# Kernel optimization log

Measured on AMD Instinct MI355X. Metric: run time of the kernel, lower is better.

## Reference

```python
import jax, jax.numpy as jnp
import numpy as np

D_MAIN = 256
D_INT = 512
N_FEAT = 128
N_CLASSES = 10
B = 1024
N_CAND = 100000
CTX = 96
EPS = 1e-5


def layer_norm(x, scale, bias):
    m = jnp.mean(x, axis=-1, keepdims=True)
    v = jnp.var(x, axis=-1, keepdims=True)
    return (x - m) / jnp.sqrt(v + EPS) * scale + bias


def setup_inputs() -> dict:
    key = jax.random.key(0)
    ks = jax.random.split(key, 16)

    def lin_w(k, fi, fo):
        return jax.random.uniform(k, (fi, fo), minval=-1.0, maxval=1.0, dtype=jnp.float32) / np.sqrt(fi)

    def lin_b(k, fi, fo):
        return jax.random.uniform(k, (fo,), minval=-1.0, maxval=1.0, dtype=jnp.float32) / np.sqrt(fi)

    return {
        "x_num": jax.random.normal(ks[0], (B, N_FEAT), dtype=jnp.float32),
        "cand_num": jax.random.normal(ks[1], (N_CAND, N_FEAT), dtype=jnp.float32),
        "cand_y": jax.random.randint(ks[2], (N_CAND,), 0, N_CLASSES),
        "context_size": CTX,
        # input linear (forward_E with encoder_n_blocks=0)
        "W_lin": lin_w(ks[3], N_FEAT, D_MAIN), "b_lin": lin_b(ks[3], N_FEAT, D_MAIN),
        # K projection
        "W_K": lin_w(ks[4], D_MAIN, D_MAIN), "b_K": lin_b(ks[4], D_MAIN, D_MAIN),
        # label embedding Y (init uniform(-1, 1) per reset_parameters)
        "Y_emb": jax.random.uniform(ks[5], (N_CLASSES, D_MAIN), minval=-1.0, maxval=1.0, dtype=jnp.float32),
        # T: Linear(d, d_int) -> ReLU -> Linear(d_int, d, bias=False)
        "T_W1": lin_w(ks[6], D_MAIN, D_INT), "T_b1": lin_b(ks[6], D_MAIN, D_INT),
        "T_W2": lin_w(ks[7], D_INT, D_MAIN),
        # predictor block (LayerNorm -> Linear -> ReLU -> Dropout -> Linear), residual
        "bp_ln_s": jnp.ones((D_MAIN,), jnp.float32), "bp_ln_b": jnp.zeros((D_MAIN,), jnp.float32),
        "bp_W1": lin_w(ks[8], D_MAIN, D_INT), "bp_b1": lin_b(ks[8], D_MAIN, D_INT),
        "bp_W2": lin_w(ks[9], D_INT, D_MAIN), "bp_b2": lin_b(ks[9], D_INT, D_MAIN),
        # head P: LayerNorm -> ReLU -> Linear(d, n_classes)
        "P_ln_s": jnp.ones((D_MAIN,), jnp.float32), "P_ln_b": jnp.zeros((D_MAIN,), jnp.float32),
        "P_W": lin_w(ks[10], D_MAIN, N_CLASSES), "P_b": lin_b(ks[10], D_MAIN, N_CLASSES),
    }


def reference(x_num, cand_num, cand_y, context_size,
              W_lin, b_lin, W_K, b_K, Y_emb, T_W1, T_b1, T_W2,
              bp_ln_s, bp_ln_b, bp_W1, bp_b1, bp_W2, bp_b2,
              P_ln_s, P_ln_b, P_W, P_b):
    # forward_E (encoder_n_blocks=0 => single Linear, normlization is None)
    x = x_num @ W_lin + b_lin                       # [B, d]
    k = x @ W_K + b_K                               # [B, d]

    # candidate keys computed under torch.no_grad in the original -> stop_gradient
    ki_all = jax.lax.stop_gradient((cand_num @ W_lin + b_lin) @ W_K + b_K)  # [N, d]

    # FAISS GpuIndexFlatL2 search: exact L2 top-k (smallest squared distance)
    d2 = (jnp.sum(k * k, axis=-1, keepdims=True)
          - 2.0 * (k @ ki_all.T)
          + jnp.sum(ki_all * ki_all, axis=-1))      # [B, N]
    _, I = jax.lax.top_k(-jax.lax.stop_gradient(d2), context_size)  # [B, C]

    ki = ki_all[I]                                  # [B, C, d]
    diff = k[:, None, :] - ki                       # [B, C, d]
    # NOTE: source computes S = -(-|k|^2 + 2 k.ki - |ki|^2) = +squared distance
    S = jnp.sum(diff * diff, axis=-1)               # [B, C]
    w = jax.nn.softmax(S, axis=-1)                  # context_dropout inactive at inference

    enc_y = Y_emb[cand_y[I]]                        # [B, C, d]
    V = enc_y + jax.nn.relu(diff @ T_W1 + T_b1) @ T_W2
    V = jnp.einsum('bc,bcd->bd', w, V)              # weighted aggregation

    x = x + V
    # predictor block (predictor_n_blocks=1)
    h = layer_norm(x, bp_ln_s, bp_ln_b)
    h = jax.nn.relu(h @ bp_W1 + bp_b1) @ bp_W2 + bp_b2
    x = x + h
    # head P
    return jax.nn.relu(layer_norm(x, P_ln_s, P_ln_b)) @ P_W + P_b
```

## Files before the change

kernel.cpp:

```cpp
#include <hip/hip_runtime.h>
#include <hip/hip_bf16.h>

#define B_ROWS   1024
#define N_FEAT   128
#define D_MAIN   256
#define D_INT    512
#define N_CAND   100000
#define CTX      96
#define N_CLS    10
#define PCHN     8192
#define N2       91808
#define RKEEP    128
#define SCAP     6144
#define MH       50000
#define SVSTRIDE 16

typedef __attribute__((ext_vector_type(8))) short bf16x8;
typedef __attribute__((ext_vector_type(4))) float f32x4;
typedef unsigned long long u64;

__device__ __forceinline__ float wsum(float v) {
    #pragma unroll
    for (int o = 32; o > 0; o >>= 1) v += __shfl_down(v, o);
    return v;
}
__device__ __forceinline__ float wmax(float v) {
    #pragma unroll
    for (int o = 32; o > 0; o >>= 1) v = fmaxf(v, __shfl_down(v, o));
    return v;
}
__device__ __forceinline__ float blockSum256(float v, float* red) {
    int t = threadIdx.x;
    float s = wsum(v);
    if ((t & 63) == 0) red[t >> 6] = s;
    __syncthreads();
    s = red[0] + red[1] + red[2] + red[3];
    __syncthreads();
    return s;
}
__device__ __forceinline__ float b2f(unsigned short u) {
    return __uint_as_float(((unsigned)u) << 16);
}
__device__ __forceinline__ unsigned short f2b(float f) {
    unsigned x = __float_as_uint(f);
    return (unsigned short)((x + 0x7fff + ((x >> 16) & 1)) >> 16);
}
__device__ __forceinline__ unsigned fkey(float f) {
    unsigned u = __float_as_uint(f);
    return u ^ ((((int)u >> 31)) | 0x80000000u);
}
__device__ __forceinline__ float finv(unsigned k) {
    unsigned u = (k & 0x80000000u) ? (k ^ 0x80000000u) : ~k;
    return __uint_as_float(u);
}
#define SPLIT1(x, hv, lv) { unsigned short _h = f2b(x); hv = (short)_h; lv = (short)f2b((x) - b2f(_h)); }

__global__ __launch_bounds__(256) void encode_batch(
    const float* __restrict__ xn, const float* __restrict__ Wl, const float* __restrict__ bl,
    const float* __restrict__ Wk, const float* __restrict__ bk,
    float* __restrict__ xout, float* __restrict__ kout, float* __restrict__ knorm)
{
    int b = blockIdx.x, t = threadIdx.x;
    __shared__ float si[128], sx[256], red[4];
    if (t < 128) si[t] = xn[b * N_FEAT + t];
    __syncthreads();
    float a = bl[t];
    for (int i = 0; i < 128; ++i) a += si[i] * Wl[i * D_MAIN + t];
    xout[b * D_MAIN + t] = a;
    sx[t] = a;
    __syncthreads();
    float a2 = bk[t];
    for (int i = 0; i < 256; ++i) a2 += sx[i] * Wk[i * D_MAIN + t];
    kout[b * D_MAIN + t] = a2;
    float s = blockSum256(a2 * a2, red);
    if (t == 0) knorm[b] = s;
}

template<bool WRITE_BF16>
__global__ __launch_bounds__(256) void gemm_split3(
    const float* __restrict__ A,
    const unsigned short* __restrict__ Bh,
    const unsigned short* __restrict__ Bl,
    const float* __restrict__ bias,
    float* __restrict__ Cf,
    unsigned short* __restrict__ Cbf,
    int M, int N, int K)
{
    __shared__ __align__(16) short Ash[4096], Asl[4096], Bsh[4096], Bsl[4096];
    const int t = threadIdx.x;
    const int bm = blockIdx.x * 128, bn = blockIdx.y * 128;
    const int wave = t >> 6, lane = t & 63;
    const int wm = (wave >> 1) * 64, wn = (wave & 1) * 64;
    const int lr = lane & 15, lkg = lane >> 4;
    f32x4 acc[4][4] = {};
    const int row0 = t >> 2, kg0 = t & 3;
    const int row1 = row0 + 64;
    const int p0 = ((kg0 + (row0 >> 2)) & 3) ^ (row0 & 3);
    const int p1 = ((kg0 + (row1 >> 2)) & 3) ^ (row1 & 3);
    const int gm0 = bm + row0, gm1 = bm + row1;
    const int n0r = bn + row0, n1r = bn + row1;

    float4 u00, u01, u10, u11;
    bf16x8 b0h, b0l, b1h, b1l;
    auto prefetch = [&](int kq) {
        float4 z4 = make_float4(0.f, 0.f, 0.f, 0.f); bf16x8 z = {};
        u00 = z4; u01 = z4; u10 = z4; u11 = z4;
        b0h = z; b0l = z; b1h = z; b1l = z;
        if (gm0 < M) {
            const float* ap = A + (size_t)gm0 * K + kq + kg0 * 8;
            u00 = *(const float4*)ap; u01 = *(const float4*)(ap + 4);
        }
        if (gm1 < M) {
            const float* ap = A + (size_t)gm1 * K + kq + kg0 * 8;
            u10 = *(const float4*)ap; u11 = *(const float4*)(ap + 4);
        }
        if (n0r < N) {
            b0h = *(const bf16x8*)(Bh + (size_t)n0r * K + kq + kg0 * 8);
            b0l = *(const bf16x8*)(Bl + (size_t)n0r * K + kq + kg0 * 8);
        }
        if (n1r < N) {
            b1h = *(const bf16x8*)(Bh + (size_t)n1r * K + kq + kg0 * 8);
            b1l = *(const bf16x8*)(Bl + (size_t)n1r * K + kq + kg0 * 8);
        }
    };
    prefetch(0);

    for (int k0 = 0; k0 < K; k0 += 32) {
        bf16x8 a0h, a0l, a1h, a1l;
        SPLIT1(u00.x, a0h[0], a0l[0]); SPLIT1(u00.y, a0h[1], a0l[1]);
        SPLIT1(u00.z, a0h[2], a0l[2]); SPLIT1(u00.w, a0h[3], a0l[3]);
        SPLIT1(u01.x, a0h[4], a0l[4]); SPLIT1(u01.y, a0h[5], a0l[5]);
        SPLIT1(u01.z, a0h[6], a0l[6]); SPLIT1(u01.w, a0h[7], a0l[7]);
        SPLIT1(u10.x, a1h[0], a1l[0]); SPLIT1(u10.y, a1h[1], a1l[1]);
        SPLIT1(u10.z, a1h[2], a1l[2]); SPLIT1(u10.w, a1h[3], a1l[3]);
        SPLIT1(u11.x, a1h[4], a1l[4]); SPLIT1(u11.y, a1h[5], a1l[5]);
        SPLIT1(u11.z, a1h[6], a1l[6]); SPLIT1(u11.w, a1h[7], a1l[7]);
        __syncthreads();
        *(bf16x8*)&Ash[(row0 * 4 + p0) * 8] = a0h;
        *(bf16x8*)&Asl[(row0 * 4 + p0) * 8] = a0l;
        *(bf16x8*)&Ash[(row1 * 4 + p1) * 8] = a1h;
        *(bf16x8*)&Asl[(row1 * 4 + p1) * 8] = a1l;
        *(bf16x8*)&Bsh[(row0 * 4 + p0) * 8] = b0h;
        *(bf16x8*)&Bsl[(row0 * 4 + p0) * 8] = b0l;
        *(bf16x8*)&Bsh[(row1 * 4 + p1) * 8] = b1h;
        *(bf16x8*)&Bsl[(row1 * 4 + p1) * 8] = b1l;
        if (k0 + 32 < K) prefetch(k0 + 32);
        __syncthreads();
        bf16x8 ah[4], al[4], bh[4], blo[4];
        #pragma unroll
        for (int m = 0; m < 4; ++m) {
            int r = wm + m * 16 + lr;
            int p = ((lkg + (r >> 2)) & 3) ^ (r & 3);
            ah[m] = *(const bf16x8*)&Ash[(r * 4 + p) * 8];
            al[m] = *(const bf16x8*)&Asl[(r * 4 + p) * 8];
        }
        #pragma unroll
        for (int n = 0; n < 4; ++n) {
            int r = wn + n * 16 + lr;
            int p = ((lkg + (r >> 2)) & 3) ^ (r & 3);
            bh[n] = *(const bf16x8*)&Bsh[(r * 4 + p) * 8];
            blo[n] = *(const bf16x8*)&Bsl[(r * 4 + p) * 8];
        }
        #pragma unroll
        for (int m = 0; m < 4; ++m)
            #pragma unroll
            for (int n = 0; n < 4; ++n) {
                acc[m][n] = __builtin_amdgcn_mfma_f32_16x16x32_bf16(al[m], bh[n], acc[m][n], 0, 0, 0);
                acc[m][n] = __builtin_amdgcn_mfma_f32_16x16x32_bf16(ah[m], blo[n], acc[m][n], 0, 0, 0);
                acc[m][n] = __builtin_amdgcn_mfma_f32_16x16x32_bf16(ah[m], bh[n], acc[m][n], 0, 0, 0);
            }
    }
    #pragma unroll
    for (int m = 0; m < 4; ++m) {
        #pragma unroll
        for (int n = 0; n < 4; ++n) {
            f32x4 a = acc[m][n];
            int gcol = bn + wn + n * 16 + lr;
            if (gcol >= N) continue;
            float bv = bias[gcol];
            #pragma unroll
            for (int r = 0; r < 4; ++r) {
                int grow = bm + wm + m * 16 + lkg * 4 + r;
                if (grow >= M) continue;
                float v = a[r] + bv;
                Cf[(size_t)grow * N + gcol] = v;
                if (WRITE_BF16) Cbf[(size_t)grow * N + gcol] = f2b(v);
            }
        }
    }
}

template<bool RELU, bool OUT_BF16>
__global__ __launch_bounds__(256) void gemm_bf16(
    const unsigned short* __restrict__ A,
    const unsigned short* __restrict__ Bt,
    const float* __restrict__ bias,
    void* __restrict__ C, int M, int N, int K)
{
    __shared__ __align__(16) short As[4096];
    __shared__ __align__(16) short Bs[2048];
    const int t = threadIdx.x;
    const int bm = blockIdx.x * 128, bn = blockIdx.y * 64;
    const int wave = t >> 6, lane = t & 63;
    const int wm = (wave >> 1) * 64, wn = (wave & 1) * 32;
    const int lr = lane & 15, lkg = lane >> 4;
    f32x4 acc[4][2] = {};
    const int row0 = t >> 2, kg0 = t & 3;
    const int row1 = row0 + 64;
    const int p0 = ((kg0 + (row0 >> 2)) & 3) ^ (row0 & 3);
    const int p1 = ((kg0 + (row1 >> 2)) & 3) ^ (row1 & 3);
    const int gm0 = bm + row0, gm1 = bm + row1;
    const int nB = bn + row0;

    bf16x8 a0, a1, b0;
    auto prefetch = [&](int kq) {
        bf16x8 z = {};
        a0 = z; a1 = z; b0 = z;
        if (gm0 < M) a0 = *(const bf16x8*)(A + (size_t)gm0 * K + kq + kg0 * 8);
        if (gm1 < M) a1 = *(const bf16x8*)(A + (size_t)gm1 * K + kq + kg0 * 8);
        if (row0 < 64 && nB < N) b0 = *(const bf16x8*)(Bt + (size_t)nB * K + kq + kg0 * 8);
    };
    prefetch(0);

    for (int k0 = 0; k0 < K; k0 += 32) {
        __syncthreads();
        *(bf16x8*)&As[(row0 * 4 + p0) * 8] = a0;
        *(bf16x8*)&As[(row1 * 4 + p1) * 8] = a1;
        if (row0 < 64) *(bf16x8*)&Bs[(row0 * 4 + p0) * 8] = b0;
        if (k0 + 32 < K) prefetch(k0 + 32);
        __syncthreads();
        bf16x8 bfr[2];
        #pragma unroll
        for (int n = 0; n < 2; ++n) {
            int r = wn + n * 16 + lr;
            int p = ((lkg + (r >> 2)) & 3) ^ (r & 3);
            bfr[n] = *(const bf16x8*)&Bs[(r * 4 + p) * 8];
        }
        #pragma unroll
        for (int m = 0; m < 4; ++m) {
            int r = wm + m * 16 + lr;
            int p = ((lkg + (r >> 2)) & 3) ^ (r & 3);
            bf16x8 af = *(const bf16x8*)&As[(r * 4 + p) * 8];
            #pragma unroll
            for (int n = 0; n < 2; ++n)
                acc[m][n] = __builtin_amdgcn_mfma_f32_16x16x32_bf16(
                    af, bfr[n], acc[m][n], 0, 0, 0);
        }
    }
    #pragma unroll
    for (int m = 0; m < 4; ++m) {
        #pragma unroll
        for (int n = 0; n < 2; ++n) {
            f32x4 a = acc[m][n];
            int gcol = bn + wn + n * 16 + lr;
            if (gcol >= N) continue;
            float bv = bias ? bias[gcol] : 0.f;
            #pragma unroll
            for (int r = 0; r < 4; ++r) {
                int grow = bm + wm + m * 16 + lkg * 4 + r;
                if (grow >= M) continue;
                float v = a[r] + bv;
                if (RELU) v = fmaxf(v, 0.f);
                if (OUT_BF16)
                    ((unsigned short*)C)[(size_t)grow * N + gcol] = f2b(v);
                else
                    ((float*)C)[(size_t)grow * N + gcol] = v;
            }
        }
    }
}

template<int MODE>
__global__ __launch_bounds__(256) void screen_gemm(
    const unsigned short* __restrict__ A,
    const unsigned short* __restrict__ Bt,
    float* __restrict__ scores,
    int N, int n0,
    const float* __restrict__ knrm,
    const unsigned* __restrict__ tau32, int* __restrict__ svcnt,
    u64* __restrict__ surv)
{
    __shared__ __align__(16) short As[4096];
    __shared__ __align__(16) short Bs[2048];
    const int t = threadIdx.x;
    const int bm = blockIdx.x * 128, bn = blockIdx.y * 64;
    const int wave = t >> 6, lane = t & 63;
    const int wm = (wave >> 1) * 64, wn = (wave & 1) * 32;
    const int lr = lane & 15, lkg = lane >> 4;
    f32x4 acc[4][2] = {};
    const int row0 = t >> 2, kg0 = t & 3;
    const int row1 = row0 + 64;
    const int p0 = ((kg0 + (row0 >> 2)) & 3) ^ (row0 & 3);
    const int p1 = ((kg0 + (row1 >> 2)) & 3) ^ (row1 & 3);
    const int gm0 = bm + row0, gm1 = bm + row1;
    const int nB = bn + row0;

    bf16x8 a0, a1, b0;
    auto prefetch = [&](int kq) {
        bf16x8 z = {};
        b0 = z;
        a0 = *(const bf16x8*)(A + (size_t)gm0 * D_MAIN + kq + kg0 * 8);
        a1 = *(const bf16x8*)(A + (size_t)gm1 * D_MAIN + kq + kg0 * 8);
        if (row0 < 64 && nB < N) b0 = *(const bf16x8*)(Bt + (size_t)nB * D_MAIN + kq + kg0 * 8);
    };
    prefetch(0);

    for (int k0 = 0; k0 < D_MAIN; k0 += 32) {
        __syncthreads();
        *(bf16x8*)&As[(row0 * 4 + p0) * 8] = a0;
        *(bf16x8*)&As[(row1 * 4 + p1) * 8] = a1;
        if (row0 < 64) *(bf16x8*)&Bs[(row0 * 4 + p0) * 8] = b0;
        if (k0 + 32 < D_MAIN) prefetch(k0 + 32);
        __syncthreads();
        bf16x8 bfr[2];
        #pragma unroll
        for (int n = 0; n < 2; ++n) {
            int r = wn + n * 16 + lr;
            int p = ((lkg + (r >> 2)) & 3) ^ (r & 3);
            bfr[n] = *(const bf16x8*)&Bs[(r * 4 + p) * 8];
        }
        #pragma unroll
        for (int m = 0; m < 4; ++m) {
            int r = wm + m * 16 + lr;
            int p = ((lkg + (r >> 2)) & 3) ^ (r & 3);
            bf16x8 af = *(const bf16x8*)&As[(r * 4 + p) * 8];
            #pragma unroll
            for (int n = 0; n < 2; ++n)
                acc[m][n] = __builtin_amdgcn_mfma_f32_16x16x32_bf16(
                    af, bfr[n], acc[m][n], 0, 0, 0);
        }
    }

    float knv[2];
    #pragma unroll
    for (int n = 0; n < 2; ++n) {
        int gcol = bn + wn + n * 16 + lr;
        knv[n] = (gcol < N) ? knrm[gcol] : 0.f;
    }
    if (MODE == 1) {
        #pragma unroll
        for (int m = 0; m < 4; ++m) {
            #pragma unroll
            for (int n = 0; n < 2; ++n) {
                int gcol = bn + wn + n * 16 + lr;
                if (gcol >= N) continue;
                #pragma unroll
                for (int r = 0; r < 4; ++r) {
                    int grow = bm + wm + m * 16 + lkg * 4 + r;
                    scores[(size_t)grow * PCHN + gcol] = knv[n] - 2.0f * acc[m][n][r];
                }
            }
        }
    } else {
        unsigned taur[16];
        #pragma unroll
        for (int m = 0; m < 4; ++m)
            #pragma unroll
            for (int r = 0; r < 4; ++r)
                taur[m * 4 + r] = tau32[bm + wm + m * 16 + lkg * 4 + r];
        #pragma unroll
        for (int m = 0; m < 4; ++m) {
            #pragma unroll
            for (int r = 0; r < 4; ++r) {
                int grow = bm + wm + m * 16 + lkg * 4 + r;
                #pragma unroll
                for (int n = 0; n < 2; ++n) {
                    int gcol = bn + wn + n * 16 + lr;
                    bool pass = false;
                    unsigned key = 0;
                    if (gcol < N) {
                        key = fkey(knv[n] - 2.0f * acc[m][n][r]);
                        pass = key <= taur[m * 4 + r];
                    }
                    u64 bal = __ballot(pass);
                    unsigned g16 = (unsigned)((bal >> (lkg * 16)) & 0xFFFFu);
                    if (g16) {
                        int cntp = __popc(g16);
                        int first = __ffs(g16) - 1;
                        int base = 0;
                        if (lr == first) base = atomicAdd(&svcnt[grow * SVSTRIDE], cntp);
                        base = __shfl(base, lkg * 16 + first);
                        if (pass) {
                            int p = base + __popc(g16 & ((1u << lr) - 1u));
                            if (p < SCAP)
                                surv[(size_t)grow * SCAP + p] =
                                    ((u64)key << 32) | (unsigned)(n0 + gcol);
                        }
                    }
                }
            }
        }
    }
}

__global__ __launch_bounds__(256) void cvt_f32_bf16_vec(
    const float* __restrict__ in, unsigned short* __restrict__ out, int n4)
{
    int i = blockIdx.x * 256 + threadIdx.x;
    if (i >= n4) return;
    float4 v = ((const float4*)in)[i];
    ushort4 u;
    u.x = f2b(v.x); u.y = f2b(v.y); u.z = f2b(v.z); u.w = f2b(v.w);
    ((ushort4*)out)[i] = u;
}
__global__ __launch_bounds__(256) void cvt_transpose(
    const float* __restrict__ W, unsigned short* __restrict__ Wt, int K, int N)
{
    int idx = blockIdx.x * 256 + threadIdx.x;
    if (idx >= K * N) return;
    int k = idx / N, n = idx % N;
    Wt[(size_t)n * K + k] = f2b(W[idx]);
}
__global__ __launch_bounds__(256) void cvt_split_transpose(
    const float* __restrict__ W, unsigned short* __restrict__ Wh,
    unsigned short* __restrict__ Wl, int K, int N)
{
    int idx = blockIdx.x * 256 + threadIdx.x;
    if (idx >= K * N) return;
    int k = idx / N, n = idx % N;
    float v = W[idx];
    unsigned short h = f2b(v);
    Wh[(size_t)n * K + k] = h;
    Wl[(size_t)n * K + k] = f2b(v - b2f(h));
}

__global__ __launch_bounds__(256) void rownorms(const float* __restrict__ ki,
                                                float* __restrict__ out, int M)
{
    int n = blockIdx.x * 4 + (threadIdx.x >> 6);
    int lane = threadIdx.x & 63;
    if (n >= M) return;
    float4 v = *(const float4*)(ki + (size_t)n * D_MAIN + lane * 4);
    float s = v.x * v.x + v.y * v.y + v.z * v.z + v.w * v.w;
    s = wsum(s);
    if (lane == 0) out[n] = s;
}

__device__ void bitonic512(u64* s, int t)
{
    for (int k = 2; k <= 512; k <<= 1) {
        for (int j = k >> 1; j > 0; j >>= 1) {
            __syncthreads();
            #pragma unroll
            for (int q = 0; q < 2; ++q) {
                int l = t + q * 256;
                int p = l ^ j;
                if (p > l) {
                    u64 a = s[l], bb = s[p];
                    bool up = ((l & k) == 0);
                    if ((a > bb) == up) { s[l] = bb; s[p] = a; }
                }
            }
        }
    }
    __syncthreads();
}
__device__ void bitonic1024(u64* s, int t)
{
    for (int k = 2; k <= 1024; k <<= 1) {
        for (int j = k >> 1; j > 0; j >>= 1) {
            __syncthreads();
            #pragma unroll
            for (int q = 0; q < 4; ++q) {
                int l = t + q * 256;
                int p = l ^ j;
                if (p > l) {
                    u64 a = s[l], bb = s[p];
                    bool up = ((l & k) == 0);
                    if ((a > bb) == up) { s[l] = bb; s[p] = a; }
                }
            }
        }
    }
    __syncthreads();
}

__global__ __launch_bounds__(256) void pilot_select(
    const float* __restrict__ scores, u64* __restrict__ pilotbuf,
    unsigned* __restrict__ tau32)
{
    int b = blockIdx.x, t = threadIdx.x;
    int lane = t & 63;
    __shared__ u64 s[1024];
    __shared__ int cnt;
    __shared__ u64 tauf;
    const float* row = scores + (size_t)b * PCHN;
    #pragma unroll
    for (int q = 0; q < 4; ++q) {
        int n = t + q * 256;
        s[n] = ((u64)fkey(row[n]) << 32) | (unsigned)n;
    }
    __syncthreads();
    bitonic1024(s, t);
    if (t == 0) { cnt = 128; tauf = s[127]; }
    #pragma unroll
    for (int q = 0; q < 4; ++q) { int n = t + q * 256; if (n >= 128) s[n] = ~0ULL; }
    __syncthreads();
    for (int base = 1024; base < PCHN; base += 1024) {
        u64 tau = tauf;
        int n = base + t * 4;
        float4 v = *(const float4*)(row + n);
        #pragma unroll
        for (int j = 0; j < 4; ++j) {
            float x = (&v.x)[j];
            u64 e = ((u64)fkey(x) << 32) | (unsigned)(n + j);
            bool pass = e < tau;
            u64 m = __ballot(pass);
            if (m) {
                int bs = 0;
                if (lane == 0) bs = atomicAdd(&cnt, (int)__popcll(m));
                bs = __shfl(bs, 0);
                if (pass) {
                    int p = bs + (int)__popcll(m & ((1ULL << lane) - 1ULL));
                    if (p < 1024) s[p] = e;
                }
            }
        }
        __syncthreads();
        if (cnt > 512) {
            bitonic1024(s, t);
            if (t == 0) { cnt = 128; tauf = s[127]; }
            #pragma unroll
            for (int q = 0; q < 4; ++q) { int n2 = t + q * 256; if (n2 >= 128) s[n2] = ~0ULL; }
        }
        __syncthreads();
    }
    bitonic1024(s, t);
    if (t < 128) pilotbuf[(size_t)b * 128 + t] = s[t];
    if (t == 0) tau32[b] = (unsigned)(s[127] >> 32);
}

__global__ __launch_bounds__(128) void init_surv(
    const u64* __restrict__ pilotbuf, u64* __restrict__ surv, int* __restrict__ svcnt)
{
    int b = blockIdx.x, t = threadIdx.x;
    surv[(size_t)b * SCAP + t] = pilotbuf[(size_t)b * 128 + t];
    if (t == 0) svcnt[b * SVSTRIDE] = 128;
}

__global__ __launch_bounds__(256) void final_select(
    const u64* __restrict__ surv, const int* __restrict__ svcnt,
    int* __restrict__ refI)
{
    int b = blockIdx.x, t = threadIdx.x;
    int lane = t & 63;
    __shared__ u64 s[1024];
    __shared__ int cnt;
    __shared__ u64 tauf;
    int total = svcnt[b * SVSTRIDE]; if (total > SCAP) total = SCAP;
    const u64* rowp = surv + (size_t)b * SCAP;
    #pragma unroll
    for (int q = 0; q < 4; ++q) {
        int n = t + q * 256;
        s[n] = (n < total) ? rowp[n] : ~0ULL;
    }
    __syncthreads();
    bitonic1024(s, t);
    if (t == 0) { cnt = 128; tauf = s[127]; }
    #pragma unroll
    for (int q = 0; q < 4; ++q) { int n = t + q * 256; if (n >= 128) s[n] = ~0ULL; }
    __syncthreads();
    for (int base = 1024; base < total; base += 1024) {
        u64 tau = tauf;
        int n = base + t * 4;
        #pragma unroll
        for (int j = 0; j < 4; ++j) {
            u64 e = (n + j < total) ? rowp[n + j] : ~0ULL;
            bool pass = e < tau;
            u64 m = __ballot(pass);
            if (m) {
                int bs = 0;
                if (lane == 0) bs = atomicAdd(&cnt, (int)__popcll(m));
                bs = __shfl(bs, 0);
                if (pass) {
                    int p = bs + (int)__popcll(m & ((1ULL << lane) - 1ULL));
                    if (p < 1024) s[p] = e;
                }
            }
        }
        __syncthreads();
        if (cnt > 512) {
            bitonic1024(s, t);
            if (t == 0) { cnt = 128; tauf = s[127]; }
            #pragma unroll
            for (int q = 0; q < 4; ++q) { int n2 = t + q * 256; if (n2 >= 128) s[n2] = ~0ULL; }
        }
        __syncthreads();
    }
    bitonic1024(s, t);
    if (t < RKEEP) refI[b * RKEEP + t] = (int)(unsigned)(s[t] & 0xffffffffULL);
}

__global__ __launch_bounds__(256) void refine(
    const float* __restrict__ kmat, const float* __restrict__ kiall,
    const float* __restrict__ knorm, const float* __restrict__ kinorm,
    const int* __restrict__ refI, int* __restrict__ Ifin, float* __restrict__ Sbuf)
{
    int b = blockIdx.x, t = threadIdx.x;
    int w = t >> 6, lane = t & 63;
    __shared__ float kk[256];
    __shared__ u64 s[512];
    kk[t] = kmat[b * D_MAIN + t];
    s[t] = ~0ULL; s[t + 256] = ~0ULL;
    __syncthreads();
    float kn = knorm[b];
    for (int sv = w; sv < RKEEP; sv += 4) {
        int n = refI[b * RKEEP + sv];
        float4 a = *(const float4*)&kk[lane * 4];
        float4 bb = ((const float4*)(kiall + (size_t)n * D_MAIN))[lane];
        float d = a.x * bb.x + a.y * bb.y + a.z * bb.z + a.w * bb.w;
        d = wsum(d);
        if (lane == 0) {
            float d2 = kn + kinorm[n] - 2.f * d;
            s[sv] = ((u64)fkey(d2) << 32) | (unsigned)n;
        }
    }
    __syncthreads();
    bitonic512(s, t);
    if (t < CTX) {
        u64 e = s[t];
        Ifin[b * CTX + t] = (int)(unsigned)(e & 0xffffffffULL);
        Sbuf[b * CTX + t] = finv((unsigned)(e >> 32));
    }
}

__global__ __launch_bounds__(64) void gather_diff_bf(
    const float* __restrict__ kmat, const float* __restrict__ kiall,
    const int* __restrict__ I, unsigned short* __restrict__ diffb)
{
    int bc = blockIdx.x;
    int b = bc / CTX;
    int t = threadIdx.x;
    int idx = I[bc];
    float4 kv = ((const float4*)(kmat + (size_t)b * D_MAIN))[t];
    float4 iv = ((const float4*)(kiall + (size_t)idx * D_MAIN))[t];
    ushort4 u;
    u.x = f2b(kv.x - iv.x); u.y = f2b(kv.y - iv.y);
    u.z = f2b(kv.z - iv.z); u.w = f2b(kv.w - iv.w);
    ((ushort4*)(diffb + (size_t)bc * D_MAIN))[t] = u;
}

__global__ __launch_bounds__(128) void softmax96(const float* __restrict__ S,
                                                 float* __restrict__ w)
{
    int b = blockIdx.x, t = threadIdx.x;
    __shared__ float rm[2], rs[2];
    float v = (t < CTX) ? S[b * CTX + t] : -__builtin_inff();
    float m = wmax(v);
    if ((t & 63) == 0) rm[t >> 6] = m;
    __syncthreads();
    m = fmaxf(rm[0], rm[1]);
    float e = (t < CTX) ? expf(v - m) : 0.f;
    float ss = wsum(e);
    if ((t & 63) == 0) rs[t >> 6] = ss;
    __syncthreads();
    float Z = rs[0] + rs[1];
    if (t < CTX) w[b * CTX + t] = e / Z;
}

__global__ __launch_bounds__(256) void aggregate(
    const float* __restrict__ w, const int* __restrict__ I,
    const int* __restrict__ cand_y, const float* __restrict__ Yemb,
    const float* __restrict__ mlp, const float* __restrict__ x,
    float* __restrict__ x2)
{
    int b = blockIdx.x, t = threadIdx.x;
    __shared__ float ws[CTX];
    __shared__ int lab[CTX];
    if (t < CTX) {
        ws[t] = w[b * CTX + t];
        lab[t] = cand_y[I[b * CTX + t]];
    }
    __syncthreads();
    float acc = 0.f;
    for (int c = 0; c < CTX; ++c) {
        acc += ws[c] * (Yemb[lab[c] * D_MAIN + t] + mlp[((size_t)b * CTX + c) * D_MAIN + t]);
    }
    x2[b * D_MAIN + t] = x[b * D_MAIN + t] + acc;
}

__global__ __launch_bounds__(256) void predictor_head(
    const float* __restrict__ x2,
    const float* __restrict__ lns, const float* __restrict__ lnb,
    const float* __restrict__ W1, const float* __restrict__ b1,
    const float* __restrict__ W2, const float* __restrict__ b2,
    const float* __restrict__ plns, const float* __restrict__ plnb,
    const float* __restrict__ PW, const float* __restrict__ Pb,
    float* __restrict__ out)
{
    int b = blockIdx.x, t = threadIdx.x;
    __shared__ float ln1[256], hdn[512], red[4];
    float xv = x2[b * D_MAIN + t];
    float s1 = blockSum256(xv, red);
    float s2 = blockSum256(xv * xv, red);
    float mean = s1 * (1.f / 256.f);
    float var = s2 * (1.f / 256.f) - mean * mean;
    float rstd = rsqrtf(var + 1e-5f);
    ln1[t] = (xv - mean) * rstd * lns[t] + lnb[t];
    __syncthreads();
    #pragma unroll
    for (int rep = 0; rep < 2; ++rep) {
        int j = t + rep * 256;
        float a = b1[j];
        for (int i = 0; i < 256; ++i) a += ln1[i] * W1[i * D_INT + j];
        hdn[j] = fmaxf(a, 0.f);
    }
    __syncthreads();
    float a3 = b2[t];
    for (int i = 0; i < 512; ++i) a3 += hdn[i] * W2[i * D_MAIN + t];
    float x3 = xv + a3;
    float s3 = blockSum256(x3, red);
    float s4 = blockSum256(x3 * x3, red);
    float m2 = s3 * (1.f / 256.f);
    float v2 = s4 * (1.f / 256.f) - m2 * m2;
    float r2 = rsqrtf(v2 + 1e-5f);
    float rv = fmaxf((x3 - m2) * r2 * plns[t] + plnb[t], 0.f);
    __syncthreads();
    ln1[t] = rv;
    __syncthreads();
    if (t < N_CLS) {
        float a = Pb[t];
        for (int i = 0; i < 256; ++i) a += ln1[i] * PW[i * N_CLS + t];
        out[b * N_CLS + t] = a;
    }
}

extern "C" void kernel_launch(void* const* d_in, const int* in_sizes, int n_in,
                              void* d_out, int out_size, void* d_ws, size_t ws_size,
                              hipStream_t stream)
{
    (void)in_sizes; (void)n_in; (void)out_size; (void)ws_size;
    const float* x_num   = (const float*)d_in[0];
    const float* cand    = (const float*)d_in[1];
    const int*   cand_y  = (const int*)d_in[2];
    const float* W_lin   = (const float*)d_in[4];
    const float* b_lin   = (const float*)d_in[5];
    const float* W_K     = (const float*)d_in[6];
    const float* b_K     = (const float*)d_in[7];
    const float* Y_emb   = (const float*)d_in[8];
    const float* T_W1    = (const float*)d_in[9];
    const float* T_b1    = (const float*)d_in[10];
    const float* T_W2    = (const float*)d_in[11];
    const float* bp_ln_s = (const float*)d_in[12];
    const float* bp_ln_b = (const float*)d_in[13];
    const float* bp_W1   = (const float*)d_in[14];
    const float* bp_b1   = (const float*)d_in[15];
    const float* bp_W2   = (const float*)d_in[16];
    const float* bp_b2   = (const float*)d_in[17];
    const float* P_ln_s  = (const float*)d_in[18];
    const float* P_ln_b  = (const float*)d_in[19];
    const float* P_W     = (const float*)d_in[20];
    const float* P_b     = (const float*)d_in[21];
    float* outp = (float*)d_out;

    char* ws = (char*)d_ws;
    float* kiall  = (float*)(ws + 0);
    unsigned short* hidden = (unsigned short*)(ws + 0);
    unsigned short* ki_bf = (unsigned short*)(ws + 102400000);
    unsigned short* diffb = (unsigned short*)(ws + 102400000);
    float* mlpbuf = (float*)(ws + 102400000);
    float* hcand  = (float*)(ws + 153600000);
    float* scores = (float*)(ws + 153600000);
    u64*   surv   = (u64*)(ws + 153600000);
    const size_t T = 204800000;
    float* xbuf   = (float*)(ws + T + 0);
    float* kbuf   = (float*)(ws + T + 1048576);
    float* x2buf  = (float*)(ws + T + 2097152);
    float* knorm  = (float*)(ws + T + 3145728);
    float* kinorm = (float*)(ws + T + 3149824);
    unsigned short* k_bf = (unsigned short*)(ws + T + 3551232);
    unsigned short* Wlh  = (unsigned short*)(ws + T + 4075520);
    unsigned short* Wll  = (unsigned short*)(ws + T + 4141056);
    unsigned short* Wkh  = (unsigned short*)(ws + T + 4206592);
    unsigned short* Wkl  = (unsigned short*)(ws + T + 4337664);
    unsigned short* W1t  = (unsigned short*)(ws + T + 4468736);
    unsigned short* W2t  = (unsigned short*)(ws + T + 4730880);
    float* Sbuf   = (float*)(ws + T + 4993024);
    float* wbuf   = (float*)(ws + T + 5386240);
    int*   refI   = (int*)(ws + T + 5779456);
    int*   Ifin   = (int*)(ws + T + 6303744);
    u64*   pilotbuf = (u64*)(ws + T + 6696960);
    unsigned* tau32 = (unsigned*)(ws + T + 7745536);
    int*   svcnt  = (int*)(ws + T + 7749632);

    encode_batch<<<B_ROWS, 256, 0, stream>>>(x_num, W_lin, b_lin, W_K, b_K,
                                             xbuf, kbuf, knorm);
    cvt_split_transpose<<<128, 256, 0, stream>>>(W_lin, Wlh, Wll, N_FEAT, D_MAIN);
    cvt_split_transpose<<<256, 256, 0, stream>>>(W_K, Wkh, Wkl, D_MAIN, D_MAIN);
    cvt_transpose<<<512, 256, 0, stream>>>(T_W1, W1t, D_MAIN, D_INT);
    cvt_transpose<<<512, 256, 0, stream>>>(T_W2, W2t, D_INT, D_MAIN);
    cvt_f32_bf16_vec<<<256, 256, 0, stream>>>(kbuf, k_bf, B_ROWS * D_MAIN / 4);
    for (int h = 0; h < 2; ++h) {
        gemm_split3<false><<<dim3(391, 2), 256, 0, stream>>>(
            cand + (size_t)h * MH * N_FEAT, Wlh, Wll, b_lin,
            hcand, nullptr, MH, D_MAIN, N_FEAT);
        gemm_split3<true><<<dim3(391, 2), 256, 0, stream>>>(
            hcand, Wkh, Wkl, b_K,
            kiall + (size_t)h * MH * D_MAIN, ki_bf + (size_t)h * MH * D_MAIN,
            MH, D_MAIN, D_MAIN);
    }
    rownorms<<<25000, 256, 0, stream>>>(kiall, kinorm, N_CAND);
    screen_gemm<1><<<dim3(8, PCHN / 64), 256, 0, stream>>>(
        k_bf, ki_bf, scores, PCHN, 0, kinorm, nullptr, nullptr, nullptr);
    pilot_select<<<B_ROWS, 256, 0, stream>>>(scores, pilotbuf, tau32);
    init_surv<<<B_ROWS, 128, 0, stream>>>(pilotbuf, surv, svcnt);
    screen_gemm<2><<<dim3(8, (N2 + 63) / 64), 256, 0, stream>>>(
        k_bf, ki_bf + (size_t)PCHN * D_MAIN, nullptr, N2, PCHN,
        kinorm + PCHN, tau32, svcnt, surv);
    final_select<<<B_ROWS, 256, 0, stream>>>(surv, svcnt, refI);
    refine<<<B_ROWS, 256, 0, stream>>>(kbuf, kiall, knorm, kinorm, refI, Ifin, Sbuf);
    softmax96<<<B_ROWS, 128, 0, stream>>>(Sbuf, wbuf);
    gather_diff_bf<<<B_ROWS * CTX, 64, 0, stream>>>(kbuf, kiall, Ifin, diffb);
    gemm_bf16<true, true><<<dim3(768, 8), 256, 0, stream>>>(
        diffb, W1t, T_b1, hidden, B_ROWS * CTX, D_INT, D_MAIN);
    gemm_bf16<false, false><<<dim3(768, 4), 256, 0, stream>>>(
        hidden, W2t, nullptr, mlpbuf, B_ROWS * CTX, D_MAIN, D_INT);
    aggregate<<<B_ROWS, 256, 0, stream>>>(wbuf, Ifin, cand_y, Y_emb, mlpbuf,
                                          xbuf, x2buf);
    predictor_head<<<B_ROWS, 256, 0, stream>>>(x2buf, bp_ln_s, bp_ln_b,
                                               bp_W1, bp_b1, bp_W2, bp_b2,
                                               P_ln_s, P_ln_b, P_W, P_b, outp);
}
```

Before: 936.2 us.

## Fold input and K projections into one fused weight for candidate encoding

Precomputes W_lin@W_K and b_lin@W_K+b_K on device, so the candidate keys come from a single 128-K split-bf16 GEMM instead of two chained GEMMs with an fp32 intermediate. This removes the hcand write and read and about two thirds of the candidate-encoding FLOPs. The split3 GEMM tile narrows to 128x64, and the bf16 GEMMs drop a row guard on B loads. Reassociating the product changes rounding slightly, which could in rare cases reorder near-tie neighbours in the top-k.

```diff
diff --git a/kernel.cpp b/kernel.cpp
--- a/kernel.cpp
+++ b/kernel.cpp
@@ -12,7 +12,6 @@
 #define N2       91808
 #define RKEEP    128
 #define SCAP     6144
-#define MH       50000
 #define SVSTRIDE 16
 
 typedef __attribute__((ext_vector_type(8))) short bf16x8;
@@ -74,6 +73,32 @@
     kout[b * D_MAIN + t] = a2;
     float s = blockSum256(a2 * a2, red);
     if (t == 0) knorm[b] = s;
+}
+
+__global__ __launch_bounds__(256) void fuse_weights(
+    const float* __restrict__ Wl, const float* __restrict__ Wk,
+    const float* __restrict__ bl, const float* __restrict__ bk,
+    float* __restrict__ Wf, float* __restrict__ bf)
+{
+    int i = blockIdx.x, t = threadIdx.x;
+    __shared__ float row[256];
+    if (i < 128) {
+        if (t < 128) row[t] = 0.f;
+        row[t % 256] = 0.f;
+        __syncthreads();
+        if (t < 256) {  }
+        row[t] = Wl[i * D_MAIN + t];
+        __syncthreads();
+        float a = 0.f;
+        for (int k = 0; k < 256; ++k) a += row[k] * Wk[k * D_MAIN + t];
+        Wf[i * D_MAIN + t] = a;
+    } else {
+        row[t] = bl[t];
+        __syncthreads();
+        float a = bk[t];
+        for (int k = 0; k < 256; ++k) a += row[k] * Wk[k * D_MAIN + t];
+        bf[t] = a;
+    }
 }
 
 template<bool WRITE_BF16>
@@ -86,26 +111,27 @@
     unsigned short* __restrict__ Cbf,
     int M, int N, int K)
 {
-    __shared__ __align__(16) short Ash[4096], Asl[4096], Bsh[4096], Bsl[4096];
+    __shared__ __align__(16) short Ash[4096], Asl[4096];
+    __shared__ __align__(16) short Bsh[2048], Bsl[2048];
     const int t = threadIdx.x;
-    const int bm = blockIdx.x * 128, bn = blockIdx.y * 128;
+    const int bm = blockIdx.x * 128, bn = blockIdx.y * 64;
     const int wave = t >> 6, lane = t & 63;
-    const int wm = (wave >> 1) * 64, wn = (wave & 1) * 64;
+    const int wm = (wave >> 1) * 64, wn = (wave & 1) * 32;
     const int lr = lane & 15, lkg = lane >> 4;
-    f32x4 acc[4][4] = {};
+    f32x4 acc[4][2] = {};
     const int row0 = t >> 2, kg0 = t & 3;
     const int row1 = row0 + 64;
     const int p0 = ((kg0 + (row0 >> 2)) & 3) ^ (row0 & 3);
     const int p1 = ((kg0 + (row1 >> 2)) & 3) ^ (row1 & 3);
     const int gm0 = bm + row0, gm1 = bm + row1;
-    const int n0r = bn + row0, n1r = bn + row1;
+    const int nB = bn + row0;
 
     float4 u00, u01, u10, u11;
-    bf16x8 b0h, b0l, b1h, b1l;
+    bf16x8 bh0, bl0;
     auto prefetch = [&](int kq) {
         float4 z4 = make_float4(0.f, 0.f, 0.f, 0.f); bf16x8 z = {};
         u00 = z4; u01 = z4; u10 = z4; u11 = z4;
-        b0h = z; b0l = z; b1h = z; b1l = z;
+        bh0 = z; bl0 = z;
         if (gm0 < M) {
             const float* ap = A + (size_t)gm0 * K + kq + kg0 * 8;
             u00 = *(const float4*)ap; u01 = *(const float4*)(ap + 4);
@@ -114,13 +140,9 @@
             const float* ap = A + (size_t)gm1 * K + kq + kg0 * 8;
             u10 = *(const float4*)ap; u11 = *(const float4*)(ap + 4);
         }
-        if (n0r < N) {
-            b0h = *(const bf16x8*)(Bh + (size_t)n0r * K + kq + kg0 * 8);
-            b0l = *(const bf16x8*)(Bl + (size_t)n0r * K + kq + kg0 * 8);
-        }
-        if (n1r < N) {
-            b1h = *(const bf16x8*)(Bh + (size_t)n1r * K + kq + kg0 * 8);
-            b1l = *(const bf16x8*)(Bl + (size_t)n1r * K + kq + kg0 * 8);
+        if (nB < N) {
+            bh0 = *(const bf16x8*)(Bh + (size_t)nB * K + kq + kg0 * 8);
+            bl0 = *(const bf16x8*)(Bl + (size_t)nB * K + kq + kg0 * 8);
         }
     };
     prefetch(0);
@@ -140,40 +162,36 @@
         *(bf16x8*)&Asl[(row0 * 4 + p0) * 8] = a0l;
         *(bf16x8*)&Ash[(row1 * 4 + p1) * 8] = a1h;
         *(bf16x8*)&Asl[(row1 * 4 + p1) * 8] = a1l;
-        *(bf16x8*)&Bsh[(row0 * 4 + p0) * 8] = b0h;
-        *(bf16x8*)&Bsl[(row0 * 4 + p0) * 8] = b0l;
-        *(bf16x8*)&Bsh[(row1 * 4 + p1) * 8] = b1h;
-        *(bf16x8*)&Bsl[(row1 * 4 + p1) * 8] = b1l;
+        *(bf16x8*)&Bsh[(row0 * 4 + p0) * 8] = bh0;
+        *(bf16x8*)&Bsl[(row0 * 4 + p0) * 8] = bl0;
         if (k0 + 32 < K) prefetch(k0 + 32);
         __syncthreads();
-        bf16x8 ah[4], al[4], bh[4], blo[4];
+        bf16x8 bfh[2], bfl[2];
+        #pragma unroll
+        for (int n = 0; n < 2; ++n) {
+            int r = wn + n * 16 + lr;
+            int p = ((lkg + (r >> 2)) & 3) ^ (r & 3);
+            bfh[n] = *(const bf16x8*)&Bsh[(r * 4 + p) * 8];
+            bfl[n] = *(const bf16x8*)&Bsl[(r * 4 + p) * 8];
+        }
         #pragma unroll
         for (int m = 0; m < 4; ++m) {
             int r = wm + m * 16 + lr;
             int p = ((lkg + (r >> 2)) & 3) ^ (r & 3);
-            ah[m] = *(const bf16x8*)&Ash[(r * 4 + p) * 8];
-            al[m] = *(const bf16x8*)&Asl[(r * 4 + p) * 8];
-        }
-        #pragma unroll
-        for (int n = 0; n < 4; ++n) {
-            int r = wn + n * 16 + lr;
-            int p = ((lkg + (r >> 2)) & 3) ^ (r & 3);
-            bh[n] = *(const bf16x8*)&Bsh[(r * 4 + p) * 8];
-            blo[n] = *(const bf16x8*)&Bsl[(r * 4 + p) * 8];
-        }
-        #pragma unroll
-        for (int m = 0; m < 4; ++m)
-            #pragma unroll
-            for (int n = 0; n < 4; ++n) {
-                acc[m][n] = __builtin_amdgcn_mfma_f32_16x16x32_bf16(al[m], bh[n], acc[m][n], 0, 0, 0);
-                acc[m][n] = __builtin_amdgcn_mfma_f32_16x16x32_bf16(ah[m], blo[n], acc[m][n], 0, 0, 0);
-                acc[m][n] = __builtin_amdgcn_mfma_f32_16x16x32_bf16(ah[m], bh[n], acc[m][n], 0, 0, 0);
+            bf16x8 ah = *(const bf16x8*)&Ash[(r * 4 + p) * 8];
+            bf16x8 al = *(const bf16x8*)&Asl[(r * 4 + p) * 8];
+            #pragma unroll
+            for (int n = 0; n < 2; ++n) {
+                acc[m][n] = __builtin_amdgcn_mfma_f32_16x16x32_bf16(al, bfh[n], acc[m][n], 0, 0, 0);
+                acc[m][n] = __builtin_amdgcn_mfma_f32_16x16x32_bf16(ah, bfl[n], acc[m][n], 0, 0, 0);
+                acc[m][n] = __builtin_amdgcn_mfma_f32_16x16x32_bf16(ah, bfh[n], acc[m][n], 0, 0, 0);
             }
+        }
     }
     #pragma unroll
     for (int m = 0; m < 4; ++m) {
         #pragma unroll
-        for (int n = 0; n < 4; ++n) {
+        for (int n = 0; n < 2; ++n) {
             f32x4 a = acc[m][n];
             int gcol = bn + wn + n * 16 + lr;
             if (gcol >= N) continue;
@@ -218,7 +236,7 @@
         a0 = z; a1 = z; b0 = z;
         if (gm0 < M) a0 = *(const bf16x8*)(A + (size_t)gm0 * K + kq + kg0 * 8);
         if (gm1 < M) a1 = *(const bf16x8*)(A + (size_t)gm1 * K + kq + kg0 * 8);
-        if (row0 < 64 && nB < N) b0 = *(const bf16x8*)(Bt + (size_t)nB * K + kq + kg0 * 8);
+        if (nB < N) b0 = *(const bf16x8*)(Bt + (size_t)nB * K + kq + kg0 * 8);
     };
     prefetch(0);
 
@@ -226,7 +244,7 @@
         __syncthreads();
         *(bf16x8*)&As[(row0 * 4 + p0) * 8] = a0;
         *(bf16x8*)&As[(row1 * 4 + p1) * 8] = a1;
-        if (row0 < 64) *(bf16x8*)&Bs[(row0 * 4 + p0) * 8] = b0;
+        *(bf16x8*)&Bs[(row0 * 4 + p0) * 8] = b0;
         if (k0 + 32 < K) prefetch(k0 + 32);
         __syncthreads();
         bf16x8 bfr[2];
@@ -301,7 +319,7 @@
         b0 = z;
         a0 = *(const bf16x8*)(A + (size_t)gm0 * D_MAIN + kq + kg0 * 8);
         a1 = *(const bf16x8*)(A + (size_t)gm1 * D_MAIN + kq + kg0 * 8);
-        if (row0 < 64 && nB < N) b0 = *(const bf16x8*)(Bt + (size_t)nB * D_MAIN + kq + kg0 * 8);
+        if (nB < N) b0 = *(const bf16x8*)(Bt + (size_t)nB * D_MAIN + kq + kg0 * 8);
     };
     prefetch(0);
 
@@ -309,7 +327,7 @@
         __syncthreads();
         *(bf16x8*)&As[(row0 * 4 + p0) * 8] = a0;
         *(bf16x8*)&As[(row1 * 4 + p1) * 8] = a1;
-        if (row0 < 64) *(bf16x8*)&Bs[(row0 * 4 + p0) * 8] = b0;
+        *(bf16x8*)&Bs[(row0 * 4 + p0) * 8] = b0;
         if (k0 + 32 < D_MAIN) prefetch(k0 + 32);
         __syncthreads();
         bf16x8 bfr[2];
@@ -759,7 +777,6 @@
     unsigned short* ki_bf = (unsigned short*)(ws + 102400000);
     unsigned short* diffb = (unsigned short*)(ws + 102400000);
     float* mlpbuf = (float*)(ws + 102400000);
-    float* hcand  = (float*)(ws + 153600000);
     float* scores = (float*)(ws + 153600000);
     u64*   surv   = (u64*)(ws + 153600000);
     const size_t T = 204800000;
@@ -769,10 +786,10 @@
     float* knorm  = (float*)(ws + T + 3145728);
     float* kinorm = (float*)(ws + T + 3149824);
     unsigned short* k_bf = (unsigned short*)(ws + T + 3551232);
-    unsigned short* Wlh  = (unsigned short*)(ws + T + 4075520);
-    unsigned short* Wll  = (unsigned short*)(ws + T + 4141056);
-    unsigned short* Wkh  = (unsigned short*)(ws + T + 4206592);
-    unsigned short* Wkl  = (unsigned short*)(ws + T + 4337664);
+    float* Wf     = (float*)(ws + T + 4075520);
+    unsigned short* WfH = (unsigned short*)(ws + T + 4206592);
+    unsigned short* WfL = (unsigned short*)(ws + T + 4272128);
+    float* bfused = (float*)(ws + T + 4337664);
     unsigned short* W1t  = (unsigned short*)(ws + T + 4468736);
     unsigned short* W2t  = (unsigned short*)(ws + T + 4730880);
     float* Sbuf   = (float*)(ws + T + 4993024);
@@ -785,20 +802,13 @@
 
     encode_batch<<<B_ROWS, 256, 0, stream>>>(x_num, W_lin, b_lin, W_K, b_K,
                                              xbuf, kbuf, knorm);
-    cvt_split_transpose<<<128, 256, 0, stream>>>(W_lin, Wlh, Wll, N_FEAT, D_MAIN);
-    cvt_split_transpose<<<256, 256, 0, stream>>>(W_K, Wkh, Wkl, D_MAIN, D_MAIN);
+    fuse_weights<<<129, 256, 0, stream>>>(W_lin, W_K, b_lin, b_K, Wf, bfused);
+    cvt_split_transpose<<<128, 256, 0, stream>>>(Wf, WfH, WfL, N_FEAT, D_MAIN);
     cvt_transpose<<<512, 256, 0, stream>>>(T_W1, W1t, D_MAIN, D_INT);
     cvt_transpose<<<512, 256, 0, stream>>>(T_W2, W2t, D_INT, D_MAIN);
     cvt_f32_bf16_vec<<<256, 256, 0, stream>>>(kbuf, k_bf, B_ROWS * D_MAIN / 4);
-    for (int h = 0; h < 2; ++h) {
-        gemm_split3<false><<<dim3(391, 2), 256, 0, stream>>>(
-            cand + (size_t)h * MH * N_FEAT, Wlh, Wll, b_lin,
-            hcand, nullptr, MH, D_MAIN, N_FEAT);
-        gemm_split3<true><<<dim3(391, 2), 256, 0, stream>>>(
-            hcand, Wkh, Wkl, b_K,
-            kiall + (size_t)h * MH * D_MAIN, ki_bf + (size_t)h * MH * D_MAIN,
-            MH, D_MAIN, D_MAIN);
-    }
+    gemm_split3<true><<<dim3(782, 4), 256, 0, stream>>>(
+        cand, WfH, WfL, bfused, kiall, ki_bf, N_CAND, D_MAIN, N_FEAT);
     rownorms<<<25000, 256, 0, stream>>>(kiall, kinorm, N_CAND);
     screen_gemm<1><<<dim3(8, PCHN / 64), 256, 0, stream>>>(
         k_bf, ki_bf, scores, PCHN, 0, kinorm, nullptr, nullptr, nullptr);
```

Result: faster. 811.0 us (-13.4%).
